# Optimization experiments

Measured on AMD Instinct MI355X. Metric: run time of the kernel, lower is better.

The kernel has to match this reference:

```python
import jax, jax.numpy as jnp
import numpy as np


def layer_norm(x, w, b, eps=1e-5):
    mu = jnp.mean(x, axis=-1, keepdims=True)
    var = jnp.mean(jnp.square(x - mu), axis=-1, keepdims=True)
    return (x - mu) / jnp.sqrt(var + eps) * w + b


def setup_inputs() -> dict:
    B, T, S, D, K = 8, 2048, 2048, 512, 3
    ks = jax.random.split(jax.random.key(0), 8)
    w_scale = 0.02  # modest init so softmax/layernorm stay in a sane range
    return {
        "x": jax.random.normal(ks[0], (B, T, D), jnp.float32),
        "enc": jax.random.normal(ks[1], (B, S, D), jnp.float32),
        "conv_w": jax.random.normal(ks[2], (2 * D, D, K), jnp.float32) * w_scale,
        "conv_b": jnp.zeros((2 * D,), jnp.float32),
        "ln1_w": jnp.ones((D,), jnp.float32),
        "ln1_b": jnp.zeros((D,), jnp.float32),
        "Wq": jax.random.normal(ks[3], (D, D), jnp.float32) * w_scale,
        "bq": jnp.zeros((D,), jnp.float32),
        "Wk": jax.random.normal(ks[4], (D, D), jnp.float32) * w_scale,
        "bk": jnp.zeros((D,), jnp.float32),
        "Wv": jax.random.normal(ks[5], (D, D), jnp.float32) * w_scale,
        "bv": jnp.zeros((D,), jnp.float32),
        "Wo": jax.random.normal(ks[6], (D, D), jnp.float32) * w_scale,
        "bo": jnp.zeros((D,), jnp.float32),
        "ln2_w": jnp.ones((D,), jnp.float32),
        "ln2_b": jnp.zeros((D,), jnp.float32),
    }


def reference(x, enc, conv_w, conv_b, ln1_w, ln1_b, Wq, bq, Wk, bk, Wv, bv, Wo, bo, ln2_w, ln2_b):
    D = x.shape[-1]
    K = conv_w.shape[-1]
    # Causal GLU: left-pad by K-1 so each output sees only past/current positions.
    xt = jnp.transpose(x, (0, 2, 1))  # [B, D, T]
    xt = jnp.pad(xt, ((0, 0), (0, 0), (K - 1, 0)))
    conv = jax.lax.conv_general_dilated(
        xt, conv_w, window_strides=(1,), padding="VALID",
        dimension_numbers=("NCH", "OIH", "NCH"))
    conv = conv + conv_b[None, :, None]
    conv = jnp.transpose(conv, (0, 2, 1))  # [B, T, 2D]
    a, g = jnp.split(conv, 2, axis=-1)
    glu = a * jax.nn.sigmoid(g)
    # residual + LN1 (dropout is identity in eval mode)
    h = layer_norm(glu + x, ln1_w, ln1_b)
    # cross-attention: bmm -> softmax -> bmm (single head)
    q = h @ Wq.T + bq            # [B, T, D]
    k = enc @ Wk.T + bk          # [B, S, D]
    v = enc @ Wv.T + bv          # [B, S, D]
    scores = jnp.einsum("btd,bsd->bts", q, k) / jnp.sqrt(jnp.float32(D))
    attn = jax.nn.softmax(scores, axis=-1)  # [B, T, S]
    ctx = jnp.einsum("bts,bsd->btd", attn, v)
    ctx = ctx @ Wo.T + bo
    out = layer_norm(h + ctx, ln2_w, ln2_b)
    return out, attn
```

## Files before the change

### kernel.cpp

```cpp
#include <hip/hip_runtime.h>
#include <hip/hip_bf16.h>
#include <stdint.h>


typedef unsigned short ushortT;
typedef __bf16 bf16x8 __attribute__((ext_vector_type(8)));
typedef float floatx4 __attribute__((ext_vector_type(4)));
typedef unsigned short ushort4v __attribute__((ext_vector_type(4)));
typedef unsigned short ushort8 __attribute__((ext_vector_type(8)));

__device__ __forceinline__ ushortT f2bf(float f) {
  unsigned u = __builtin_bit_cast(unsigned, f);
  u += 0x7FFFu + ((u >> 16) & 1u);
  return (ushortT)(u >> 16);
}
__device__ __forceinline__ float bf2f(ushortT u) {
  return __builtin_bit_cast(float, (unsigned)u << 16);
}

__device__ __forceinline__ void gload_lds16(const void* g, void* l) {
  __builtin_amdgcn_global_load_lds(
      (const __attribute__((address_space(1))) void*)g,
      (__attribute__((address_space(3))) void*)l, 16, 0, 0);
}

__global__ __launch_bounds__(256)
void k_f32_to_bf16v(const float* __restrict__ src, ushortT* __restrict__ dst, long n4) {
  long i = (long)blockIdx.x * 256 + threadIdx.x;
  if (i >= n4) return;
  floatx4 v = *(const floatx4*)&src[i * 4];
  ushort4v o;
#pragma unroll
  for (int j = 0; j < 4; j++) o[j] = f2bf(v[j]);
  *(ushort4v*)&dst[i * 4] = o;
}

__global__ __launch_bounds__(256)
void k_w4(const float* __restrict__ w0, const float* __restrict__ w1,
          const float* __restrict__ w2, const float* __restrict__ w3,
          ushortT* __restrict__ dst) {
  long i = (long)blockIdx.x * 256 + threadIdx.x;
  int m = (int)(i >> 16);
  long within = (i & 65535) * 4;
  const float* s = (m == 0) ? w0 : (m == 1) ? w1 : (m == 2) ? w2 : w3;
  floatx4 v = *(const floatx4*)&s[within];
  ushort4v o;
#pragma unroll
  for (int j = 0; j < 4; j++) o[j] = f2bf(v[j]);
  *(ushort4v*)&dst[(long)m * 262144 + within] = o;
}

__global__ __launch_bounds__(128)
void k_xpad(const float* __restrict__ x, ushortT* __restrict__ xp) {
  int row = blockIdx.x;
  int b = row / 2050, tp = row % 2050;
  int c = threadIdx.x * 4;
  ushort4v o = {0, 0, 0, 0};
  if (tp >= 2) {
    floatx4 v = *(const floatx4*)&x[((long)(b * 2048 + tp - 2)) * 512 + c];
#pragma unroll
    for (int j = 0; j < 4; j++) o[j] = f2bf(v[j]);
  }
  *(ushort4v*)&xp[(long)row * 512 + c] = o;
}

__global__ __launch_bounds__(256)
void k_convw(const float* __restrict__ w, ushortT* __restrict__ dst) {
  long idx = (long)blockIdx.x * 256 + threadIdx.x;
  if (idx >= 1024L * 1536) return;
  int n = (int)(idx / 1536), kk = (int)(idx % 1536);
  int tap = kk >> 9, i = kk & 511;
  int o = ((n >> 4) & 1) * 512 + (n >> 5) * 16 + (n & 15);
  dst[idx] = f2bf(w[(o * 512 + i) * 3 + tap]);
}

template<int CONV_A, int BIAS, int GLU, int WBF16, int SWAP = 0>
__global__ __launch_bounds__(256)
void k_gemm(const ushortT* __restrict__ A, long aBatch, int lda,
            const ushortT* __restrict__ Bm, long bBatch, int ldb,
            const float* __restrict__ bias, const float* __restrict__ xres,
            float* __restrict__ Cf, ushortT* __restrict__ Cb, long cBatch, int ldc,
            int Kdim, float scale)
{
  __shared__ ushortT As[128 * 32];
  __shared__ ushortT Bs[128 * 32];
  const int tid  = threadIdx.x;
  const int lane = tid & 63;
  const int wave = tid >> 6;
  const int wrow = (wave >> 1) * 64;
  const int wcol = (wave & 1) * 64;
  const int l15  = lane & 15;
  const int quad = lane >> 4;
  const long zA = (long)blockIdx.z * aBatch;
  const long zB = (long)blockIdx.z * bBatch;
  const long zC = (long)blockIdx.z * cBatch;
  const int rowBase = (SWAP ? blockIdx.y : blockIdx.x) * 128;
  const int colBase = (SWAP ? blockIdx.x : blockIdx.y) * 128;

  floatx4 zero = {0.f, 0.f, 0.f, 0.f};
  floatx4 acc[4][4];
#pragma unroll
  for (int mi = 0; mi < 4; mi++)
#pragma unroll
    for (int ni = 0; ni < 4; ni++) acc[mi][ni] = zero;

  for (int k0 = 0; k0 < Kdim; k0 += 32) {
    __syncthreads();
    {
      int ch = tid;
#pragma unroll
      for (int it = 0; it < 2; it++, ch += 256) {
        int row = ch >> 2, c8 = (ch & 3) << 3;
        if (CONV_A) {
          int gr = rowBase + row, gc = k0 + c8;
          int tap = gc >> 9, ii = gc & 511;
          int b = gr >> 11, t = gr & 2047;
          long gofs = ((long)(b * 2050 + t + tap) << 9) + ii;
          gload_lds16(A + gofs, &As[ch * 8]);
        } else {
          long gofs = zA + (long)(rowBase + row) * lda + (k0 + c8);
          gload_lds16(A + gofs, &As[ch * 8]);
        }
      }
      ch = tid;
#pragma unroll
      for (int it = 0; it < 2; it++, ch += 256) {
        int row = ch >> 2, c8 = (ch & 3) << 3;
        long gofs = zB + (long)(colBase + row) * ldb + (k0 + c8);
        gload_lds16(Bm + gofs, &Bs[ch * 8]);
      }
    }
    __syncthreads();
    bf16x8 av[4], bv[4];
#pragma unroll
    for (int mi = 0; mi < 4; mi++)
      av[mi] = *(const bf16x8*)&As[(wrow + mi * 16 + l15) * 32 + quad * 8];
#pragma unroll
    for (int ni = 0; ni < 4; ni++)
      bv[ni] = *(const bf16x8*)&Bs[(wcol + ni * 16 + l15) * 32 + quad * 8];
#pragma unroll
    for (int mi = 0; mi < 4; mi++)
#pragma unroll
      for (int ni = 0; ni < 4; ni++)
        acc[mi][ni] = __builtin_amdgcn_mfma_f32_16x16x32_bf16(av[mi], bv[ni], acc[mi][ni], 0, 0, 0);
  }

  if (GLU) {
#pragma unroll
    for (int mi = 0; mi < 4; mi++) {
#pragma unroll
      for (int ni = 0; ni < 4; ni += 2) {
        int colA = colBase + wcol + ni * 16;
        int d = (colA >> 5) * 16 + l15;
        float ba = bias[d], bg = bias[512 + d];
#pragma unroll
        for (int r = 0; r < 4; r++) {
          int grow = rowBase + wrow + mi * 16 + quad * 4 + r;
          float a = acc[mi][ni][r] + ba;
          float g = acc[mi][ni + 1][r] + bg;
          float val = a / (1.0f + __expf(-g)) + xres[(long)grow * 512 + d];
          Cf[(long)grow * 512 + d] = val;
        }
      }
    }
  } else {
#pragma unroll
    for (int mi = 0; mi < 4; mi++) {
#pragma unroll
      for (int ni = 0; ni < 4; ni++) {
        int gcol = colBase + wcol + ni * 16 + l15;
        float bcol = (BIAS == 1) ? bias[gcol] : 0.0f;
#pragma unroll
        for (int r = 0; r < 4; r++) {
          int grow = rowBase + wrow + mi * 16 + quad * 4 + r;
          float val = acc[mi][ni][r] * scale + bcol + ((BIAS == 2) ? bias[grow] : 0.0f);
          long off = zC + (long)grow * ldc + gcol;
          if (WBF16) Cb[off] = f2bf(val);
          else       Cf[off] = val;
        }
      }
    }
  }
}

__global__ __launch_bounds__(128)
void k_ln(const float* __restrict__ src, const float* __restrict__ w, const float* __restrict__ b,
          ushortT* __restrict__ outb)
{
  __shared__ float s1[2], s2[2];
  long r = blockIdx.x;
  int tid = threadIdx.x;
  floatx4 v = *(const floatx4*)&src[r * 512 + tid * 4];
  float sum = v[0] + v[1] + v[2] + v[3];
  float ssq = v[0]*v[0] + v[1]*v[1] + v[2]*v[2] + v[3]*v[3];
#pragma unroll
  for (int off = 32; off; off >>= 1) { sum += __shfl_xor(sum, off); ssq += __shfl_xor(ssq, off); }
  if ((tid & 63) == 0) { s1[tid >> 6] = sum; s2[tid >> 6] = ssq; }
  __syncthreads();
  sum = s1[0] + s1[1]; ssq = s2[0] + s2[1];
  float mu = sum * (1.0f / 512.0f);
  float var = ssq * (1.0f / 512.0f) - mu * mu;
  float rstd = rsqrtf(var + 1e-5f);
  floatx4 wv = *(const floatx4*)&w[tid * 4];
  floatx4 bv = *(const floatx4*)&b[tid * 4];
  ushort4v ob;
#pragma unroll
  for (int j = 0; j < 4; j++) ob[j] = f2bf((v[j] - mu) * rstd * wv[j] + bv[j]);
  *(ushort4v*)&outb[r * 512 + tid * 4] = ob;
}

__global__ __launch_bounds__(256)
void k_softmax(ushortT* __restrict__ logits, float* __restrict__ attn)
{
  __shared__ float sred[4];
  long r = blockIdx.x;
  ushortT* lrow = logits + r * 2048;
  float* arow = attn + r * 2048;
  int tid = threadIdx.x;
  ushort8 uv = *(const ushort8*)&lrow[tid * 8];
  float v[8];
#pragma unroll
  for (int j = 0; j < 8; j++) v[j] = bf2f(uv[j]);
  float mx = v[0];
#pragma unroll
  for (int j = 1; j < 8; j++) mx = fmaxf(mx, v[j]);
#pragma unroll
  for (int off = 32; off; off >>= 1) mx = fmaxf(mx, __shfl_xor(mx, off));
  if ((tid & 63) == 0) sred[tid >> 6] = mx;
  __syncthreads();
  mx = fmaxf(fmaxf(sred[0], sred[1]), fmaxf(sred[2], sred[3]));
  __syncthreads();
  float sum = 0.f;
#pragma unroll
  for (int j = 0; j < 8; j++) { v[j] = __expf(v[j] - mx); sum += v[j]; }
#pragma unroll
  for (int off = 32; off; off >>= 1) sum += __shfl_xor(sum, off);
  if ((tid & 63) == 0) sred[tid >> 6] = sum;
  __syncthreads();
  sum = sred[0] + sred[1] + sred[2] + sred[3];
  float inv = 1.0f / sum;
  floatx4 o0, o1;
  ushort8 ob;
#pragma unroll
  for (int j = 0; j < 8; j++) {
    float p = v[j] * inv;
    if (j < 4) o0[j] = p; else o1[j - 4] = p;
    ob[j] = f2bf(p);
  }
  *(floatx4*)&arow[tid * 8] = o0;
  *(floatx4*)&arow[tid * 8 + 4] = o1;
  *(ushort8*)&lrow[tid * 8] = ob;
}

__global__ __launch_bounds__(256)
void k_oproj_ln(const ushortT* __restrict__ ctx, const ushortT* __restrict__ Wo,
                const float* __restrict__ bo, const ushortT* __restrict__ h,
                const float* __restrict__ w, const float* __restrict__ b,
                float* __restrict__ out)
{
  __shared__ ushortT As[32 * 32];
  __shared__ ushortT Bs[512 * 32];
  __shared__ float psum[4][32], pssq[4][32];
  const int tid = threadIdx.x, lane = tid & 63, wave = tid >> 6;
  const int l15 = lane & 15, quad = lane >> 4;
  const int rowBase = blockIdx.x * 32;

  floatx4 zero = {0.f, 0.f, 0.f, 0.f};
  floatx4 acc[2][8];
#pragma unroll
  for (int mi = 0; mi < 2; mi++)
#pragma unroll
    for (int ni = 0; ni < 8; ni++) acc[mi][ni] = zero;

  for (int k0 = 0; k0 < 512; k0 += 32) {
    __syncthreads();
    if (tid < 128)
      gload_lds16(ctx + (long)(rowBase + (tid >> 2)) * 512 + k0 + ((tid & 3) << 3), &As[tid * 8]);
#pragma unroll
    for (int it = 0; it < 8; it++) {
      int ch = tid + it * 256;
      gload_lds16(Wo + (long)(ch >> 2) * 512 + k0 + ((ch & 3) << 3), &Bs[ch * 8]);
    }
    __syncthreads();
    bf16x8 av[2], bv[8];
#pragma unroll
    for (int mi = 0; mi < 2; mi++)
      av[mi] = *(const bf16x8*)&As[(mi * 16 + l15) * 32 + quad * 8];
#pragma unroll
    for (int ni = 0; ni < 8; ni++)
      bv[ni] = *(const bf16x8*)&Bs[(wave * 128 + ni * 16 + l15) * 32 + quad * 8];
#pragma unroll
    for (int mi = 0; mi < 2; mi++)
#pragma unroll
      for (int ni = 0; ni < 8; ni++)
        acc[mi][ni] = __builtin_amdgcn_mfma_f32_16x16x32_bf16(av[mi], bv[ni], acc[mi][ni], 0, 0, 0);
  }

  float lnw[8], lnb[8], bov[8];
#pragma unroll
  for (int ni = 0; ni < 8; ni++) {
    int col = wave * 128 + ni * 16 + l15;
    bov[ni] = bo[col]; lnw[ni] = w[col]; lnb[ni] = b[col];
  }
#pragma unroll
  for (int mi = 0; mi < 2; mi++) {
#pragma unroll
    for (int r = 0; r < 4; r++) {
      long grow = rowBase + mi * 16 + quad * 4 + r;
      float ps = 0.f, pq = 0.f;
#pragma unroll
      for (int ni = 0; ni < 8; ni++) {
        int col = wave * 128 + ni * 16 + l15;
        float val = acc[mi][ni][r] + bov[ni] + bf2f(h[grow * 512 + col]);
        acc[mi][ni][r] = val;
        ps += val; pq += val * val;
      }
#pragma unroll
      for (int off = 1; off < 16; off <<= 1) { ps += __shfl_xor(ps, off); pq += __shfl_xor(pq, off); }
      if (l15 == 0) { int rl = mi * 16 + quad * 4 + r; psum[wave][rl] = ps; pssq[wave][rl] = pq; }
    }
  }
  __syncthreads();
#pragma unroll
  for (int mi = 0; mi < 2; mi++) {
#pragma unroll
    for (int r = 0; r < 4; r++) {
      int rl = mi * 16 + quad * 4 + r;
      float S = psum[0][rl] + psum[1][rl] + psum[2][rl] + psum[3][rl];
      float Q = pssq[0][rl] + pssq[1][rl] + pssq[2][rl] + pssq[3][rl];
      float mu = S * (1.0f / 512.0f);
      float rstd = rsqrtf(Q * (1.0f / 512.0f) - mu * mu + 1e-5f);
      long grow = rowBase + rl;
#pragma unroll
      for (int ni = 0; ni < 8; ni++) {
        int col = wave * 128 + ni * 16 + l15;
        out[grow * 512 + col] = (acc[mi][ni][r] - mu) * rstd * lnw[ni] + lnb[ni];
      }
    }
  }
}

extern "C" void kernel_launch(void* const* d_in, const int* in_sizes, int n_in,
                              void* d_out, int out_size, void* d_ws, size_t ws_size,
                              hipStream_t stream)
{
  const float* x      = (const float*)d_in[0];
  const float* enc    = (const float*)d_in[1];
  const float* conv_w = (const float*)d_in[2];
  const float* conv_b = (const float*)d_in[3];
  const float* ln1_w  = (const float*)d_in[4];
  const float* ln1_b  = (const float*)d_in[5];
  const float* Wq     = (const float*)d_in[6];
  const float* bq     = (const float*)d_in[7];
  const float* Wk     = (const float*)d_in[8];
  const float* bk     = (const float*)d_in[9];
  const float* Wv     = (const float*)d_in[10];
  const float* bv     = (const float*)d_in[11];
  const float* Wo     = (const float*)d_in[12];
  const float* bo     = (const float*)d_in[13];
  const float* ln2_w  = (const float*)d_in[14];
  const float* ln2_b  = (const float*)d_in[15];

  const long BT = 16384, Dd = 512, S = 2048, TT = 2048;
  float* out  = (float*)d_out;
  float* attn = out + BT * Dd;

  char* p = (char*)d_ws;
  auto alloc = [&](size_t bytes) { char* r = p; p += (bytes + 255) & ~255UL; return r; };
  float*   hglu  = (float*)alloc(BT * Dd * 4);
  ushortT* xpad  = (ushortT*)alloc(8L * 2050 * 512 * 2);
  ushortT* encbf = (ushortT*)alloc(BT * Dd * 2);
  ushortT* hbf   = (ushortT*)alloc(BT * Dd * 2);
  ushortT* qbf   = (ushortT*)alloc(BT * Dd * 2);
  ushortT* kbf   = (ushortT*)alloc(BT * Dd * 2);
  ushortT* vT    = (ushortT*)alloc(Dd * BT * 2);
  ushortT* ctxbf = (ushortT*)alloc(BT * Dd * 2);
  ushortT* sl    = (ushortT*)alloc(BT * S * 2);
  ushortT* Wcbf  = (ushortT*)alloc(1024L * 1536 * 2);
  ushortT* wall  = (ushortT*)alloc(4L * 262144 * 2);
  ushortT* Wqbf = wall, *Wkbf = wall + 262144, *Wvbf = wall + 2 * 262144, *Wobf = wall + 3 * 262144;

  k_xpad<<<8 * 2050, 128, 0, stream>>>(x, xpad);
  k_f32_to_bf16v<<<(BT * Dd / 4 + 255) / 256, 256, 0, stream>>>(enc, encbf, BT * Dd / 4);
  k_convw<<<(1024 * 1536 + 255) / 256, 256, 0, stream>>>(conv_w, Wcbf);
  k_w4<<<1024, 256, 0, stream>>>(Wq, Wk, Wv, Wo, wall);

  k_gemm<1, 1, 1, 0><<<dim3(128, 8), 256, 0, stream>>>(
      xpad, 0, 0, Wcbf, 0, 1536, conv_b, x, hglu, nullptr, 0, 512, 1536, 1.0f);
  k_ln<<<16384, 128, 0, stream>>>(hglu, ln1_w, ln1_b, hbf);

  k_gemm<0, 1, 0, 1><<<dim3(128, 4), 256, 0, stream>>>(
      hbf, 0, 512, Wqbf, 0, 512, bq, nullptr, nullptr, qbf, 0, 512, 512, 1.0f);
  k_gemm<0, 1, 0, 1><<<dim3(128, 4), 256, 0, stream>>>(
      encbf, 0, 512, Wkbf, 0, 512, bk, nullptr, nullptr, kbf, 0, 512, 512, 1.0f);
  k_gemm<0, 2, 0, 1><<<dim3(4, 128), 256, 0, stream>>>(
      Wvbf, 0, 512, encbf, 0, 512, bv, nullptr, nullptr, vT, 0, 16384, 512, 1.0f);

  k_gemm<0, 0, 0, 1><<<dim3(16, 16, 8), 256, 0, stream>>>(
      qbf, TT * Dd, 512, kbf, S * Dd, 512, nullptr, nullptr,
      nullptr, sl, TT * S, 2048, 512, 0.04419417382415922f);
  k_softmax<<<16384, 256, 0, stream>>>(sl, attn);

  k_gemm<0, 0, 0, 1, 1><<<dim3(4, 16, 8), 256, 0, stream>>>(
      sl, TT * S, 2048, vT, TT, 16384, nullptr, nullptr,
      nullptr, ctxbf, TT * Dd, 512, 2048, 1.0f);

  k_oproj_ln<<<512, 256, 0, stream>>>(ctxbf, Wobf, bo, hbf, ln2_w, ln2_b, out);
}
```

Measured before the change: 589.2 us.

## Add 256x256-tile 512-thread GEMM kernel and merge Q/K projections

Adds a new GEMM kernel with 256x256 output tiles, 8 waves per block, a double-buffered XOR-swizzled LDS stage filled by direct global-to-LDS loads, and s_setprio around the MFMA bursts. It replaces the older GEMM for the conv/GLU, QK-scores and attn·V products, and fuses the Q and K projections into one launch using a dual-pointer z dimension. The larger tiles are meant to raise data reuse per LDS byte and cut launch count. In exchange each block uses far more registers and LDS, which lowers occupancy and leaves fewer blocks for the smaller grids, e.g. only 128 blocks for the attn·V product.

Result: faster. 526.9 us (-10.6%).

```diff
diff --git a/kernel.cpp b/kernel.cpp
--- a/kernel.cpp
+++ b/kernel.cpp
@@ -183,6 +183,170 @@
   }
 }
 
+template<int CONV_A, int GLU, int BIAS, int WBF16, int DUALZ, int SWAP>
+__global__ __launch_bounds__(512)
+void k_gemm256(const ushortT* __restrict__ A, const ushortT* __restrict__ A2, int lda, long aBatch,
+               const ushortT* __restrict__ Bm, const ushortT* __restrict__ Bm2, int ldb, long bBatch,
+               const float* __restrict__ bias, const float* __restrict__ bias2,
+               const float* __restrict__ xres,
+               float* __restrict__ Cf, ushortT* __restrict__ Cb, ushortT* __restrict__ Cb2,
+               long cBatch, int ldc, int Kdim, float scale)
+{
+  __shared__ ushortT lds[2][2 * 16384];
+
+  const int tid  = threadIdx.x;
+  const int lane = tid & 63;
+  const int wave = tid >> 6;
+  const int wr   = wave >> 2;
+  const int wc   = wave & 3;
+  const int l15  = lane & 15;
+  const int quad = lane >> 4;
+
+  const ushortT* Ap = A;
+  const ushortT* Bp = Bm;
+  const float* biasP = bias;
+  ushortT* CbP = Cb;
+  if (DUALZ && blockIdx.z) { Ap = A2; Bp = Bm2; biasP = bias2; CbP = Cb2; }
+  const long zA = DUALZ ? 0 : (long)blockIdx.z * aBatch;
+  const long zB = DUALZ ? 0 : (long)blockIdx.z * bBatch;
+  const long zC = DUALZ ? 0 : (long)blockIdx.z * cBatch;
+  const int rowBase = (SWAP ? blockIdx.y : blockIdx.x) * 256;
+  const int colBase = (SWAP ? blockIdx.x : blockIdx.y) * 256;
+
+  auto STAGE = [&](int t) {
+    ushortT* sA = lds[t & 1];
+    ushortT* sB = sA + 16384;
+    const int k0 = t << 6;
+#pragma unroll
+    for (int l = 0; l < 4; l++) {
+      int idx = l * 512 + tid;
+      int row = idx >> 3;
+      int ck  = ((tid & 7) ^ (row & 7)) << 3;
+      if (CONV_A) {
+        int gr = rowBase + row;
+        int gc = k0 + ck;
+        int tap = gc >> 9, ii = gc & 511;
+        int b = gr >> 11, tt = gr & 2047;
+        long gofs = ((long)(b * 2050 + tt + tap) << 9) + ii;
+        gload_lds16(Ap + gofs, sA + idx * 8);
+      } else {
+        long gofs = zA + (long)(rowBase + row) * lda + (k0 + ck);
+        gload_lds16(Ap + gofs, sA + idx * 8);
+      }
+    }
+#pragma unroll
+    for (int l = 0; l < 4; l++) {
+      int idx = l * 512 + tid;
+      int row = idx >> 3;
+      int ck  = ((tid & 7) ^ (row & 7)) << 3;
+      long gofs = zB + (long)(colBase + row) * ldb + (k0 + ck);
+      gload_lds16(Bp + gofs, sB + idx * 8);
+    }
+  };
+
+  auto LD = [&](const ushortT* s, int r, int c) -> bf16x8 {
+    return *(const bf16x8*)&s[r * 64 + ((c ^ (r & 7)) << 3)];
+  };
+
+  floatx4 zero = {0.f, 0.f, 0.f, 0.f};
+  floatx4 acc[8][4];
+#pragma unroll
+  for (int mi = 0; mi < 8; mi++)
+#pragma unroll
+    for (int ni = 0; ni < 4; ni++) acc[mi][ni] = zero;
+
+  const int NT = Kdim >> 6;
+  STAGE(0);
+  STAGE(1);
+
+  for (int t = 0; t < NT; t++) {
+    if (t < NT - 1) asm volatile("s_waitcnt vmcnt(8)" ::: "memory");
+    else            asm volatile("s_waitcnt vmcnt(0)" ::: "memory");
+    __builtin_amdgcn_s_barrier();
+
+    const ushortT* sA = lds[t & 1];
+    const ushortT* sB = sA + 16384;
+
+    bf16x8 av[4][2], bv[4][2];
+#pragma unroll
+    for (int ni = 0; ni < 4; ni++)
+#pragma unroll
+      for (int ks = 0; ks < 2; ks++)
+        bv[ni][ks] = LD(sB, wc * 64 + ni * 16 + l15, ks * 4 + quad);
+#pragma unroll
+    for (int mi = 0; mi < 4; mi++)
+#pragma unroll
+      for (int ks = 0; ks < 2; ks++)
+        av[mi][ks] = LD(sA, wr * 128 + mi * 16 + l15, ks * 4 + quad);
+
+    __builtin_amdgcn_s_setprio(1);
+#pragma unroll
+    for (int mi = 0; mi < 4; mi++)
+#pragma unroll
+      for (int ni = 0; ni < 4; ni++)
+#pragma unroll
+        for (int ks = 0; ks < 2; ks++)
+          acc[mi][ni] = __builtin_amdgcn_mfma_f32_16x16x32_bf16(av[mi][ks], bv[ni][ks], acc[mi][ni], 0, 0, 0);
+    __builtin_amdgcn_s_setprio(0);
+
+#pragma unroll
+    for (int mi = 0; mi < 4; mi++)
+#pragma unroll
+      for (int ks = 0; ks < 2; ks++)
+        av[mi][ks] = LD(sA, wr * 128 + 64 + mi * 16 + l15, ks * 4 + quad);
+
+    __builtin_amdgcn_s_setprio(1);
+#pragma unroll
+    for (int mi = 0; mi < 4; mi++)
+#pragma unroll
+      for (int ni = 0; ni < 4; ni++)
+#pragma unroll
+        for (int ks = 0; ks < 2; ks++)
+          acc[4 + mi][ni] = __builtin_amdgcn_mfma_f32_16x16x32_bf16(av[mi][ks], bv[ni][ks], acc[4 + mi][ni], 0, 0, 0);
+    __builtin_amdgcn_s_setprio(0);
+
+    __builtin_amdgcn_s_barrier();
+    if (t + 2 < NT) STAGE(t + 2);
+  }
+
+  if (GLU) {
+#pragma unroll
+    for (int mi = 0; mi < 8; mi++) {
+#pragma unroll
+      for (int ni = 0; ni < 4; ni += 2) {
+        int colA = colBase + wc * 64 + ni * 16;
+        int d = (colA >> 5) * 16 + l15;
+        float ba = biasP[d], bg = biasP[512 + d];
+#pragma unroll
+        for (int r = 0; r < 4; r++) {
+          int grow = rowBase + wr * 128 + mi * 16 + quad * 4 + r;
+          float a = acc[mi][ni][r] + ba;
+          float g = acc[mi][ni + 1][r] + bg;
+          float val = a / (1.0f + __expf(-g)) + xres[(long)grow * 512 + d];
+          Cf[(long)grow * 512 + d] = val;
+        }
+      }
+    }
+  } else {
+#pragma unroll
+    for (int mi = 0; mi < 8; mi++) {
+#pragma unroll
+      for (int ni = 0; ni < 4; ni++) {
+        int gcol = colBase + wc * 64 + ni * 16 + l15;
+        float bcol = BIAS ? biasP[gcol] : 0.0f;
+#pragma unroll
+        for (int r = 0; r < 4; r++) {
+          int grow = rowBase + wr * 128 + mi * 16 + quad * 4 + r;
+          float val = acc[mi][ni][r] * scale + bcol;
+          long off = zC + (long)grow * ldc + gcol;
+          if (WBF16) CbP[off] = f2bf(val);
+          else       Cf[off] = val;
+        }
+      }
+    }
+  }
+}
+
 __global__ __launch_bounds__(128)
 void k_ln(const float* __restrict__ src, const float* __restrict__ w, const float* __restrict__ b,
           ushortT* __restrict__ outb)
@@ -385,25 +549,28 @@
   k_convw<<<(1024 * 1536 + 255) / 256, 256, 0, stream>>>(conv_w, Wcbf);
   k_w4<<<1024, 256, 0, stream>>>(Wq, Wk, Wv, Wo, wall);
 
-  k_gemm<1, 1, 1, 0><<<dim3(128, 8), 256, 0, stream>>>(
-      xpad, 0, 0, Wcbf, 0, 1536, conv_b, x, hglu, nullptr, 0, 512, 1536, 1.0f);
+  k_gemm256<1, 1, 0, 0, 0, 0><<<dim3(64, 4, 1), 512, 0, stream>>>(
+      xpad, nullptr, 0, 0, Wcbf, nullptr, 1536, 0,
+      conv_b, nullptr, x, hglu, nullptr, nullptr, 0, 512, 1536, 1.0f);
   k_ln<<<16384, 128, 0, stream>>>(hglu, ln1_w, ln1_b, hbf);
 
-  k_gemm<0, 1, 0, 1><<<dim3(128, 4), 256, 0, stream>>>(
-      hbf, 0, 512, Wqbf, 0, 512, bq, nullptr, nullptr, qbf, 0, 512, 512, 1.0f);
-  k_gemm<0, 1, 0, 1><<<dim3(128, 4), 256, 0, stream>>>(
-      encbf, 0, 512, Wkbf, 0, 512, bk, nullptr, nullptr, kbf, 0, 512, 512, 1.0f);
+  k_gemm256<0, 0, 1, 1, 1, 0><<<dim3(64, 2, 2), 512, 0, stream>>>(
+      hbf, encbf, 512, 0, Wqbf, Wkbf, 512, 0,
+      bq, bk, nullptr, nullptr, qbf, kbf, 0, 512, 512, 1.0f);
+
   k_gemm<0, 2, 0, 1><<<dim3(4, 128), 256, 0, stream>>>(
       Wvbf, 0, 512, encbf, 0, 512, bv, nullptr, nullptr, vT, 0, 16384, 512, 1.0f);
 
-  k_gemm<0, 0, 0, 1><<<dim3(16, 16, 8), 256, 0, stream>>>(
-      qbf, TT * Dd, 512, kbf, S * Dd, 512, nullptr, nullptr,
-      nullptr, sl, TT * S, 2048, 512, 0.04419417382415922f);
+  k_gemm256<0, 0, 0, 1, 0, 0><<<dim3(8, 8, 8), 512, 0, stream>>>(
+      qbf, nullptr, 512, TT * Dd, kbf, nullptr, 512, S * Dd,
+      nullptr, nullptr, nullptr, nullptr, sl, nullptr,
+      TT * S, 2048, 512, 0.04419417382415922f);
   k_softmax<<<16384, 256, 0, stream>>>(sl, attn);
 
-  k_gemm<0, 0, 0, 1, 1><<<dim3(4, 16, 8), 256, 0, stream>>>(
-      sl, TT * S, 2048, vT, TT, 16384, nullptr, nullptr,
-      nullptr, ctxbf, TT * Dd, 512, 2048, 1.0f);
+  k_gemm256<0, 0, 0, 1, 0, 1><<<dim3(2, 8, 8), 512, 0, stream>>>(
+      sl, nullptr, 2048, TT * S, vT, nullptr, 16384, TT,
+      nullptr, nullptr, nullptr, nullptr, ctxbf, nullptr,
+      TT * Dd, 512, 2048, 1.0f);
 
   k_oproj_ln<<<512, 256, 0, stream>>>(ctxbf, Wobf, bo, hbf, ln2_w, ln2_b, out);
 }
```
